# Kernel optimization log

Measured on AMD Instinct MI355X. Metric: run time of the kernel, lower is better.

The kernel has to match this reference:

```python
import jax, jax.numpy as jnp
import numpy as np

EPS = 1e-5
NUM_HEADS = 16


def activation_quant(x):
    # 8-bit activation quant with straight-through estimator
    scale = 127.0 / jnp.clip(jnp.max(jnp.abs(x), axis=-1, keepdims=True), 1e-5, None)
    y = jnp.clip(jnp.round(x * scale), -128.0, 127.0) / scale
    return x + jax.lax.stop_gradient(y - x)


def weight_quant(w):
    # ternary {-1,0,1} weight quant with STE
    scale = 1.0 / jnp.clip(jnp.mean(jnp.abs(w)), 1e-5, None)
    wq = jnp.clip(jnp.round(w * scale), -1.0, 1.0) / scale
    return w + jax.lax.stop_gradient(wq - w)


def bitlinear(x, w):
    # F.layer_norm(x, x.shape[1:]): normalize over ALL dims except batch, no affine
    axes = tuple(range(1, x.ndim))
    mu = jnp.mean(x, axis=axes, keepdims=True)
    var = jnp.var(x, axis=axes, keepdims=True)
    xn = (x - mu) * jax.lax.rsqrt(var + EPS)
    return jnp.einsum('bnd,od->bno', activation_quant(xn), weight_quant(w))


def layer_norm(x, gamma, beta):
    mu = jnp.mean(x, axis=-1, keepdims=True)
    var = jnp.var(x, axis=-1, keepdims=True)
    return (x - mu) * jax.lax.rsqrt(var + EPS) * gamma + beta


def setup_inputs() -> dict:
    key = jax.random.key(0)
    k0, k1, k2 = jax.random.split(key, 3)
    B, N, D = 2, 2048, 1024
    return {
        't': jnp.zeros((1,), jnp.float32),
        'x': jax.random.normal(k0, (B, N, D), jnp.float32),
        'w_qkv': jax.random.normal(k1, (3 * D, D), jnp.float32) * 0.02,
        'w_out': jax.random.normal(k2, (D, D), jnp.float32) * 0.02,
        'gamma': jnp.ones((D,), jnp.float32),
        'beta': jnp.zeros((D,), jnp.float32),
    }


def reference(t, x, w_qkv, w_out, gamma, beta):
    B, N, D = x.shape
    H = NUM_HEADS
    hd = D // H
    scale = hd ** -0.5
    h = layer_norm(x, gamma, beta)                     # [B,N,D]
    qkv = bitlinear(h, w_qkv).reshape(B, N, 3, H, hd)   # [B,N,3,H,hd]
    qkv = jnp.transpose(qkv, (2, 0, 3, 1, 4))           # [3,B,H,N,hd]
    q, k, v = qkv[0], qkv[1], qkv[2]
    attn = jax.nn.softmax(jnp.einsum('bhnd,bhmd->bhnm', q, k) * scale, axis=-1)
    out = jnp.einsum('bhnm,bhmd->bhnd', attn, v)        # [B,H,N,hd]
    out = jnp.transpose(out, (0, 2, 1, 3)).reshape(B, N, D)
    return bitlinear(out, w_out)
```

## Files before the change

kernel.cpp:

```cpp
#include <hip/hip_runtime.h>
#include <hip/hip_bf16.h>
#include <hip/hip_fp16.h>
#include <math.h>

typedef __hip_bfloat16 bf16;
typedef int   i32x4  __attribute__((ext_vector_type(4)));
typedef float f32x4  __attribute__((ext_vector_type(4)));
typedef float f32x16 __attribute__((ext_vector_type(16)));
typedef short bfx8   __attribute__((ext_vector_type(8)));

#define EPSV 1e-5f
#define NROWS 4096
#define DIM   1024
#define NSEQ  2048

__device__ __forceinline__ float ldv(const void* p, size_t i, int dt){
  if (dt == 0) return ((const float*)p)[i];
  if (dt == 1) return __bfloat162float(((const bf16*)p)[i]);
  return __half2float(((const __half*)p)[i]);
}

__device__ __forceinline__ void detect(const void* c0, const void* c1,
                                       int& dt, const void*& g, const void*& bta){
  unsigned u0 = *(const unsigned*)c0;
  int gfirst = (u0 != 0u) ? 1 : 0;
  g   = gfirst ? c0 : c1;
  bta = gfirst ? c1 : c0;
  unsigned short g0 = *(const unsigned short*)g;
  dt = (g0 == 0x3F80) ? 1 : ((g0 == 0x3C00) ? 2 : 0);
}

__device__ __forceinline__ float blk_sum(float v, float* sm){
  #pragma unroll
  for (int o = 32; o > 0; o >>= 1) v += __shfl_xor(v, o, 64);
  __syncthreads();
  if ((threadIdx.x & 63) == 0) sm[threadIdx.x >> 6] = v;
  __syncthreads();
  return sm[0] + sm[1] + sm[2] + sm[3];
}
__device__ __forceinline__ double blk_sum_d(double v, double* sm){
  #pragma unroll
  for (int o = 32; o > 0; o >>= 1) v += __shfl_xor(v, o, 64);
  __syncthreads();
  if ((threadIdx.x & 63) == 0) sm[threadIdx.x >> 6] = v;
  __syncthreads();
  return sm[0] + sm[1] + sm[2] + sm[3];
}
__device__ __forceinline__ float blk_max(float v, float* sm){
  #pragma unroll
  for (int o = 32; o > 0; o >>= 1) v = fmaxf(v, __shfl_xor(v, o, 64));
  __syncthreads();
  if ((threadIdx.x & 63) == 0) sm[threadIdx.x >> 6] = v;
  __syncthreads();
  return fmaxf(fmaxf(sm[0], sm[1]), fmaxf(sm[2], sm[3]));
}

__global__ __launch_bounds__(256) void ln_rows(const void* __restrict__ x,
                                               const void* __restrict__ c0,
                                               const void* __restrict__ c1,
                                               float* __restrict__ h,
                                               double* __restrict__ lnp){
  __shared__ float sm[4];
  __shared__ double smd[4];
  int dt; const void *g, *bta;
  detect(c0, c1, dt, g, bta);
  int row = blockIdx.x;
  int tid = threadIdx.x;
  float v[4]; float s = 0.f;
  float gmv[4], btv[4];
  if (dt == 0){
    float4 v4 = ((const float4*)x)[(size_t)row*256 + tid];
    v[0]=v4.x; v[1]=v4.y; v[2]=v4.z; v[3]=v4.w;
    float4 gm4 = ((const float4*)g)[tid];
    float4 bt4 = ((const float4*)bta)[tid];
    gmv[0]=gm4.x; gmv[1]=gm4.y; gmv[2]=gm4.z; gmv[3]=gm4.w;
    btv[0]=bt4.x; btv[1]=bt4.y; btv[2]=bt4.z; btv[3]=bt4.w;
  } else {
    size_t base = (size_t)row * DIM;
    #pragma unroll
    for (int i = 0; i < 4; ++i){
      v[i]   = ldv(x, base + 4*tid + i, dt);
      gmv[i] = ldv(g, 4*tid + i, dt);
      btv[i] = ldv(bta, 4*tid + i, dt);
    }
  }
  #pragma unroll
  for (int i = 0; i < 4; ++i) s += v[i];
  s = blk_sum(s, sm);
  float mu = s * (1.f/1024.f);
  float d2 = 0.f;
  #pragma unroll
  for (int i = 0; i < 4; ++i){ float d = v[i] - mu; d2 += d*d; }
  d2 = blk_sum(d2, sm);
  float rs = rsqrtf(d2 * (1.f/1024.f) + EPSV);
  float hv[4];
  #pragma unroll
  for (int i = 0; i < 4; ++i) hv[i] = (v[i]-mu)*rs*gmv[i] + btv[i];
  ((float4*)h)[(size_t)row*256 + tid] = make_float4(hv[0],hv[1],hv[2],hv[3]);
  double hs = 0.0, hq = 0.0;
  #pragma unroll
  for (int i = 0; i < 4; ++i){ hs += (double)hv[i]; hq += (double)hv[i]*(double)hv[i]; }
  hs = blk_sum_d(hs, smd);
  hq = blk_sum_d(hq, smd);
  if (tid == 0){ lnp[2*row] = hs; lnp[2*row + 1] = hq; }
}

__global__ __launch_bounds__(256) void abs_reduce_both(const void* __restrict__ wq,
                                                       const void* __restrict__ wo,
                                                       double* __restrict__ awp1,
                                                       double* __restrict__ awp2,
                                                       const void* __restrict__ c0,
                                                       const void* __restrict__ c1){
  __shared__ double smd[4];
  int dt; const void *g, *bta;
  detect(c0, c1, dt, g, bta);
  int blk = blockIdx.x;
  const void* w; int n; int nblk; int bi; double* part;
  if (blk < 512){ w = wq; n = 3*DIM*DIM; nblk = 512; bi = blk;      part = awp1; }
  else          { w = wo; n = DIM*DIM;   nblk = 128; bi = blk - 512; part = awp2; }
  double s = 0.0;
  if (dt == 0){
    const float4* w4 = (const float4*)w;
    int n4 = n >> 2;
    for (int i = bi*256 + threadIdx.x; i < n4; i += nblk*256){
      float4 v = w4[i];
      s += (double)(fabsf(v.x) + fabsf(v.y)) + (double)(fabsf(v.z) + fabsf(v.w));
    }
  } else {
    for (int i = bi*256 + threadIdx.x; i < n; i += nblk*256)
      s += (double)fabsf(ldv(w, i, dt));
  }
  s = blk_sum_d(s, smd);
  if (threadIdx.x == 0) part[bi] = s;
}

__global__ __launch_bounds__(256) void finalize1(float* acc,
                                                 const double* __restrict__ lnp,
                                                 const double* __restrict__ awp1,
                                                 const double* __restrict__ awp2){
  __shared__ double smd[4];
  int tid = threadIdx.x;
  double s0=0, q0=0, s1=0, q1=0, a1=0, a2=0;
  for (int i = tid; i < 2048; i += 256){
    s0 += lnp[2*i];          q0 += lnp[2*i + 1];
    s1 += lnp[2*(i+2048)];   q1 += lnp[2*(i+2048) + 1];
  }
  for (int i = tid; i < 512; i += 256) a1 += awp1[i];
  if (tid < 128) a2 = awp2[tid];
  s0 = blk_sum_d(s0, smd);  q0 = blk_sum_d(q0, smd);
  s1 = blk_sum_d(s1, smd);  q1 = blk_sum_d(q1, smd);
  a1 = blk_sum_d(a1, smd);  a2 = blk_sum_d(a2, smd);
  if (tid == 0){
    const double cnt = 2097152.0;
    double mu0 = s0/cnt, var0 = q0/cnt - mu0*mu0;
    double mu1 = s1/cnt, var1 = q1/cnt - mu1*mu1;
    acc[16] = (float)mu0; acc[17] = (float)(1.0 / sqrt(var0 + 1e-5));
    acc[18] = (float)mu1; acc[19] = (float)(1.0 / sqrt(var1 + 1e-5));
    acc[20] = (float)(1.0 / fmax(a1 / (3.0*1024.0*1024.0), 1e-5));
    acc[21] = (float)(1.0 / fmax(a2 / (1024.0*1024.0), 1e-5));
  }
}

__global__ __launch_bounds__(256) void finalize2(float* acc,
                                                 const double* __restrict__ atp){
  __shared__ double smd[4];
  int tid = threadIdx.x;
  double s0=0, q0=0, s1=0, q1=0;
  for (int i = tid; i < 512; i += 256){
    s0 += atp[2*i];          q0 += atp[2*i + 1];
    s1 += atp[2*(i+512)];    q1 += atp[2*(i+512) + 1];
  }
  s0 = blk_sum_d(s0, smd);  q0 = blk_sum_d(q0, smd);
  s1 = blk_sum_d(s1, smd);  q1 = blk_sum_d(q1, smd);
  if (tid == 0){
    const double cnt = 2097152.0;
    double mu0 = s0/cnt, var0 = q0/cnt - mu0*mu0;
    double mu1 = s1/cnt, var1 = q1/cnt - mu1*mu1;
    acc[22] = (float)mu0; acc[23] = (float)(1.0 / sqrt(var0 + 1e-5));
    acc[24] = (float)mu1; acc[25] = (float)(1.0 / sqrt(var1 + 1e-5));
  }
}

__global__ __launch_bounds__(256) void act_quant_i8(const float* __restrict__ buf,
                                                    signed char* __restrict__ qout,
                                                    float* __restrict__ rscale,
                                                    const float* __restrict__ acc,
                                                    int statOff){
  __shared__ float sm[4];
  int row = blockIdx.x;
  int b = row >> 11;
  float mu = acc[statOff + 2*b], rs = acc[statOff + 2*b + 1];
  int tid = threadIdx.x;
  float4 v4 = ((const float4*)buf)[(size_t)row*256 + tid];
  float v[4] = {(v4.x-mu)*rs, (v4.y-mu)*rs, (v4.z-mu)*rs, (v4.w-mu)*rs};
  float am = fmaxf(fmaxf(fabsf(v[0]), fabsf(v[1])), fmaxf(fabsf(v[2]), fabsf(v[3])));
  am = blk_max(am, sm);
  am = fmaxf(am, 1e-5f);
  float s127 = 127.f / am;
  unsigned pk = 0;
  #pragma unroll
  for (int i = 0; i < 4; ++i){
    float q = rintf(v[i] * s127);
    q = fminf(fmaxf(q, -128.f), 127.f);
    pk |= ((unsigned)(unsigned char)(signed char)q) << (8*i);
  }
  ((unsigned*)qout)[(size_t)row*256 + tid] = pk;
  if (tid == 0) rscale[row] = am * (1.f/127.f);
}

__global__ __launch_bounds__(256) void w_quant_both(const void* __restrict__ wqv,
                                                    const void* __restrict__ wov,
                                                    signed char* __restrict__ wqk,
                                                    signed char* __restrict__ wqo,
                                                    const float* __restrict__ acc,
                                                    const void* __restrict__ c0,
                                                    const void* __restrict__ c1){
  int dt; const void *g, *bta;
  detect(c0, c1, dt, g, bta);
  const int NQ4 = 786432;
  const int NT4 = 1048576;
  float s1 = acc[20], s2 = acc[21];
  if (dt == 0){
    for (int i = blockIdx.x*256 + threadIdx.x; i < NT4; i += gridDim.x*256){
      int inq = (i < NQ4);
      const float4* src = inq ? (const float4*)wqv : (const float4*)wov;
      unsigned* dst = inq ? (unsigned*)wqk : (unsigned*)wqo;
      int idx = inq ? i : (i - NQ4);
      float scale = inq ? s1 : s2;
      float4 v = src[idx];
      float vv[4] = {v.x, v.y, v.z, v.w};
      unsigned pk = 0;
      #pragma unroll
      for (int j = 0; j < 4; ++j){
        float q = rintf(vv[j] * scale);
        q = fminf(fmaxf(q, -1.f), 1.f);
        pk |= ((unsigned)(unsigned char)(signed char)q) << (8*j);
      }
      dst[idx] = pk;
    }
  } else {
    const int NQ = 3*DIM*DIM, NT = 4*DIM*DIM;
    for (int i = blockIdx.x*256 + threadIdx.x; i < NT; i += gridDim.x*256){
      int inq = (i < NQ);
      int idx = inq ? i : (i - NQ);
      float scale = inq ? s1 : s2;
      float q = rintf(ldv(inq ? wqv : wov, idx, dt) * scale);
      q = fminf(fmaxf(q, -1.f), 1.f);
      (inq ? wqk : wqo)[idx] = (signed char)q;
    }
  }
}

__global__ __launch_bounds__(256) void gemm_i8(const signed char* __restrict__ A,
                                               const signed char* __restrict__ W,
                                               const float* __restrict__ rscale,
                                               const float* __restrict__ acc, int sidx,
                                               float* __restrict__ Cf,
                                               bf16* __restrict__ Cb,
                                               int ldc, int writeBf, float q_prescale){
  __shared__ __attribute__((aligned(16))) signed char Asl[128][80];
  __shared__ __attribute__((aligned(16))) signed char Bsl[128][80];
  int tid = threadIdx.x, lane = tid & 63, w = tid >> 6;
  int wr = w >> 1, wc = w & 1;

  int nwgx = gridDim.x;
  int flat = blockIdx.y * nwgx + blockIdx.x;
  int nwg  = nwgx * gridDim.y;
  int cpx  = nwg >> 3;
  int swz  = (flat & 7) * cpx + (flat >> 3);
  int r0 = (swz / nwgx) * 128, o0 = (swz % nwgx) * 128;

  i32x4 zz = {0,0,0,0};
  i32x4 accv[4][4];
  #pragma unroll
  for (int m = 0; m < 4; ++m)
    #pragma unroll
    for (int n = 0; n < 4; ++n) accv[m][n] = zz;

  int sr0 = tid >> 2, sr1 = sr0 + 64;
  int sc  = (tid & 3) * 16;

  i32x4 a0, a1, b0, b1;
  a0 = *(const i32x4*)(A + (size_t)(r0 + sr0)*1024 + sc);
  a1 = *(const i32x4*)(A + (size_t)(r0 + sr1)*1024 + sc);
  b0 = *(const i32x4*)(W + (size_t)(o0 + sr0)*1024 + sc);
  b1 = *(const i32x4*)(W + (size_t)(o0 + sr1)*1024 + sc);

  for (int k0 = 0; k0 < 1024; k0 += 64){
    __syncthreads();
    *(i32x4*)&Asl[sr0][sc] = a0;
    *(i32x4*)&Asl[sr1][sc] = a1;
    *(i32x4*)&Bsl[sr0][sc] = b0;
    *(i32x4*)&Bsl[sr1][sc] = b1;
    __syncthreads();
    if (k0 + 64 < 1024){
      int kn = k0 + 64;
      a0 = *(const i32x4*)(A + (size_t)(r0 + sr0)*1024 + kn + sc);
      a1 = *(const i32x4*)(A + (size_t)(r0 + sr1)*1024 + kn + sc);
      b0 = *(const i32x4*)(W + (size_t)(o0 + sr0)*1024 + kn + sc);
      b1 = *(const i32x4*)(W + (size_t)(o0 + sr1)*1024 + kn + sc);
    }
    i32x4 af[4], bfr[4];
    #pragma unroll
    for (int m = 0; m < 4; ++m)
      af[m] = *(const i32x4*)&Asl[wr*64 + m*16 + (lane & 15)][(lane >> 4) * 16];
    #pragma unroll
    for (int n = 0; n < 4; ++n)
      bfr[n] = *(const i32x4*)&Bsl[wc*64 + n*16 + (lane & 15)][(lane >> 4) * 16];
    __builtin_amdgcn_s_setprio(1);
    #pragma unroll
    for (int m = 0; m < 4; ++m)
      #pragma unroll
      for (int n = 0; n < 4; ++n)
        accv[m][n] = __builtin_amdgcn_mfma_i32_16x16x64_i8(af[m], bfr[n], accv[m][n], 0, 0, 0);
    __builtin_amdgcn_s_setprio(0);
  }

  float wsc = acc[sidx];
  float cs = (o0 < 1024) ? q_prescale : 1.0f;
  float rf[4][4];
  #pragma unroll
  for (int m = 0; m < 4; ++m)
    #pragma unroll
    for (int r = 0; r < 4; ++r)
      rf[m][r] = rscale[r0 + wr*64 + m*16 + ((lane >> 4) << 2) + r] / wsc * cs;

  #pragma unroll
  for (int m = 0; m < 4; ++m)
    #pragma unroll
    for (int n = 0; n < 4; ++n)
      #pragma unroll
      for (int r = 0; r < 4; ++r){
        float val = (float)accv[m][n][r] * rf[m][r];
        size_t row = (size_t)(r0 + wr*64 + m*16 + ((lane >> 4) << 2) + r);
        int col = o0 + wc*64 + n*16 + (lane & 15);
        if (writeBf) Cb[row * ldc + col] = __float2bfloat16(val);
        else         Cf[row * ldc + col] = val;
      }
}

__global__ __launch_bounds__(128) void attn_mfma(const bf16* __restrict__ qkv,
                                                 float* __restrict__ out,
                                                 double* __restrict__ atp){
  __shared__ __attribute__((aligned(16))) unsigned short K_lds[64][64];
  __shared__ __attribute__((aligned(16))) unsigned short Vt_lds[64][64];
  __shared__ double smd[2];

  int tid = threadIdx.x, lane = tid & 63, w = tid >> 6;
  int l31 = lane & 31, hi = lane >> 5;

  int flat = blockIdx.y * 32 + blockIdx.x;
  int slot = flat & 7, idx = flat >> 3;
  int bh = slot * 4 + (idx >> 5);
  int qx = idx & 31;
  int b = bh >> 4, h = bh & 15;
  int n0 = qx * 64;
  const unsigned short* qg = (const unsigned short*)qkv;

  char* kB = (char*)K_lds;
  char* vB = (char*)Vt_lds;

  int qrow = b*NSEQ + n0 + w*32 + l31;
  bfx8 qf[4];
  #pragma unroll
  for (int kk = 0; kk < 4; ++kk)
    qf[kk] = *(const bfx8*)(qg + (size_t)qrow*3072 + h*64 + kk*16 + hi*8);

  float m_run = -INFINITY, l_run = 0.f;
  f32x16 acco[2];
  #pragma unroll
  for (int n = 0; n < 2; ++n)
    #pragma unroll
    for (int r = 0; r < 16; ++r) acco[n][r] = 0.f;

  int krow = tid & 63;
  int r2 = tid & 31, dw = tid >> 5;
  int k7 = krow & 7;

  bfx8 kc[4], vv[4];
  auto LOADT = [&](int kt){
    size_t kvb = (size_t)(b*NSEQ + kt*64);
    #pragma unroll
    for (int j = 0; j < 4; ++j)
      kc[j] = *(const bfx8*)(qg + (kvb + krow)*3072 + 1024 + h*64 + (w + 2*j)*8);
    vv[0] = *(const bfx8*)(qg + (kvb + 2*r2    )*3072 + 2048 + h*64 + dw*8);
    vv[1] = *(const bfx8*)(qg + (kvb + 2*r2 + 1)*3072 + 2048 + h*64 + dw*8);
    vv[2] = *(const bfx8*)(qg + (kvb + 2*r2    )*3072 + 2048 + h*64 + (dw+4)*8);
    vv[3] = *(const bfx8*)(qg + (kvb + 2*r2 + 1)*3072 + 2048 + h*64 + (dw+4)*8);
  };
  LOADT(0);

  for (int kt = 0; kt < NSEQ/64; ++kt){
    __syncthreads();
    #pragma unroll
    for (int j = 0; j < 4; ++j)
      *(bfx8*)(kB + krow*128 + (((w + 2*j) ^ k7) << 4)) = kc[j];
    #pragma unroll
    for (int u = 0; u < 8; ++u){
      unsigned w0 = (unsigned)(unsigned short)vv[0][u] |
                    ((unsigned)(unsigned short)vv[1][u] << 16);
      unsigned w1 = (unsigned)(unsigned short)vv[2][u] |
                    ((unsigned)(unsigned short)vv[3][u] << 16);
      *(unsigned*)(vB + (dw*8 + u)*128     + ((4*r2) ^ (u << 4))) = w0;
      *(unsigned*)(vB + ((dw+4)*8 + u)*128 + ((4*r2) ^ (u << 4))) = w1;
    }
    __syncthreads();
    if (kt + 1 < NSEQ/64) LOADT(kt + 1);

    f32x16 s0, s1;
    #pragma unroll
    for (int r = 0; r < 16; ++r){ s0[r] = 0.f; s1[r] = 0.f; }
    int q7 = l31 & 7;
    #pragma unroll
    for (int kk = 0; kk < 4; ++kk){
      bfx8 kb0 = *(const bfx8*)(kB + l31*128        + (((2*kk + hi) ^ q7) << 4));
      bfx8 kb1 = *(const bfx8*)(kB + (32 + l31)*128 + (((2*kk + hi) ^ q7) << 4));
      __builtin_amdgcn_s_setprio(1);
      s0 = __builtin_amdgcn_mfma_f32_32x32x16_bf16(kb0, qf[kk], s0, 0, 0, 0);
      s1 = __builtin_amdgcn_mfma_f32_32x32x16_bf16(kb1, qf[kk], s1, 0, 0, 0);
      __builtin_amdgcn_s_setprio(0);
    }

    float pm = s0[0];
    #pragma unroll
    for (int r = 1; r < 16; ++r) pm = fmaxf(pm, s0[r]);
    #pragma unroll
    for (int r = 0; r < 16; ++r) pm = fmaxf(pm, s1[r]);
    pm = fmaxf(pm, __shfl_xor(pm, 32, 64));
    if (__any(pm > m_run + 8.f)){
      float mnew = fmaxf(m_run, pm);
      float corr = __expf(m_run - mnew);
      m_run = mnew;
      l_run *= corr;
      #pragma unroll
      for (int r = 0; r < 16; ++r){
        float ca = __shfl(corr, (r & 3) + 8*(r >> 2) + 4*hi, 64);
        acco[0][r] *= ca; acco[1][r] *= ca;
      }
    }
    float ts = 0.f;
    #pragma unroll
    for (int r = 0; r < 16; ++r){
      s0[r] = __expf(s0[r] - m_run); ts += s0[r];
      s1[r] = __expf(s1[r] - m_run); ts += s1[r];
    }
    ts += __shfl_xor(ts, 32, 64);
    l_run += ts;

    #pragma unroll
    for (int kvb = 0; kvb < 2; ++kvb){
      const f32x16& s = kvb ? s1 : s0;
      #pragma unroll
      for (int kk2 = 0; kk2 < 2; ++kk2){
        int bse = kk2 * 8;
        unsigned wa, wb2, wc, wd;
        asm("v_cvt_pk_bf16_f32 %0, %1, %2" : "=v"(wa)  : "v"(s[bse+0]), "v"(s[bse+1]));
        asm("v_cvt_pk_bf16_f32 %0, %1, %2" : "=v"(wb2) : "v"(s[bse+4]), "v"(s[bse+5]));
        asm("v_cvt_pk_bf16_f32 %0, %1, %2" : "=v"(wc)  : "v"(s[bse+2]), "v"(s[bse+3]));
        asm("v_cvt_pk_bf16_f32 %0, %1, %2" : "=v"(wd)  : "v"(s[bse+6]), "v"(s[bse+7]));
        asm("v_permlane32_swap_b32 %0, %1" : "+v"(wa), "+v"(wb2));
        asm("v_permlane32_swap_b32 %0, %1" : "+v"(wc), "+v"(wd));
        unsigned pw[4] = {wa, wc, wb2, wd};
        bfx8 pa = *(bfx8*)pw;
        #pragma unroll
        for (int n = 0; n < 2; ++n){
          bfx8 vb = *(const bfx8*)(vB + (n*32 + l31)*128 +
                                   (((kvb*4 + kk2*2 + hi) ^ q7) << 4));
          __builtin_amdgcn_s_setprio(1);
          acco[n] = __builtin_amdgcn_mfma_f32_32x32x16_bf16(pa, vb, acco[n], 0, 0, 0);
          __builtin_amdgcn_s_setprio(0);
        }
      }
    }
  }

  float il = 1.f / l_run;
  float ila[16];
  #pragma unroll
  for (int r = 0; r < 16; ++r)
    ila[r] = __shfl(il, (r & 3) + 8*(r >> 2) + 4*hi, 64);
  double ssum = 0.0, ssq = 0.0;
  #pragma unroll
  for (int n = 0; n < 2; ++n)
    #pragma unroll
    for (int r = 0; r < 16; ++r){
      float o = acco[n][r] * ila[r];
      int orow = b*NSEQ + n0 + w*32 + (r & 3) + 8*(r >> 2) + 4*hi;
      out[(size_t)orow * DIM + h*64 + n*32 + l31] = o;
      ssum += (double)o; ssq += (double)o * (double)o;
    }
  #pragma unroll
  for (int o = 32; o > 0; o >>= 1){ ssum += __shfl_xor(ssum, o, 64); ssq += __shfl_xor(ssq, o, 64); }
  __syncthreads();
  if (lane == 0){ smd[w] = ssum; }
  __syncthreads();
  double tsum = smd[0] + smd[1];
  __syncthreads();
  if (lane == 0){ smd[w] = ssq; }
  __syncthreads();
  double tsq = smd[0] + smd[1];
  if (tid == 0){
    int bflat = bh * 32 + qx;
    atp[2*bflat] = tsum; atp[2*bflat + 1] = tsq;
  }
}

extern "C" void kernel_launch(void* const* d_in, const int* in_sizes, int n_in,
                              void* d_out, int out_size, void* d_ws, size_t ws_size,
                              hipStream_t stream) {
  int ix = -1, iwq = -1, iwo = -1, ig0 = -1, ig1 = -1;
  for (int i = 0; i < n_in; ++i){
    int s = in_sizes[i];
    if      (s == 4194304) ix  = i;
    else if (s == 3145728) iwq = i;
    else if (s == 1048576) iwo = i;
    else if (s == 1024){ if (ig0 < 0) ig0 = i; else ig1 = i; }
  }
  if (ix < 0 || iwq < 0 || iwo < 0 || ig0 < 0 || ig1 < 0){ ix=1; iwq=2; iwo=3; ig0=4; ig1=5; }
  const void* x     = d_in[ix];
  const void* w_qkv = d_in[iwq];
  const void* w_out = d_in[iwo];
  const void* g0    = d_in[ig0];
  const void* g1    = d_in[ig1];

  char* ws = (char*)d_ws;
  float*  acc     = (float*)ws;
  float*  rscale1 = (float*)(ws + 12288);
  float*  rscale2 = (float*)(ws + 28672);
  double* lnp     = (double*)(ws + 65536);
  double* awp1    = (double*)(ws + 131072);
  double* awp2    = (double*)(ws + 135168);
  double* atp     = (double*)(ws + 139264);
  float*        h      = (float*)      (ws + (1u<<20));
  signed char*  h_i8   = (signed char*)(ws + (17u<<20));
  signed char*  wqk_i8 = (signed char*)(ws + (21u<<20));
  signed char*  wqo_i8 = (signed char*)(ws + (24u<<20));
  bf16*         qkvb   = (bf16*)       (ws + (25u<<20));
  signed char*  a2_i8  = (signed char*)(ws + (49u<<20));
  float*        aout   = h;

  ln_rows<<<NROWS, 256, 0, stream>>>(x, g0, g1, h, lnp);
  abs_reduce_both<<<640, 256, 0, stream>>>(w_qkv, w_out, awp1, awp2, g0, g1);
  finalize1<<<1, 256, 0, stream>>>(acc, lnp, awp1, awp2);
  act_quant_i8<<<NROWS, 256, 0, stream>>>(h, h_i8, rscale1, acc, 16);
  w_quant_both<<<1024, 256, 0, stream>>>(w_qkv, w_out, wqk_i8, wqo_i8, acc, g0, g1);
  gemm_i8<<<dim3(24, 32), 256, 0, stream>>>(h_i8, wqk_i8, rscale1, acc, 20,
                                            nullptr, qkvb, 3072, 1, 0.125f);
  attn_mfma<<<dim3(32, 32), 128, 0, stream>>>(qkvb, aout, atp);
  finalize2<<<1, 256, 0, stream>>>(acc, atp);
  act_quant_i8<<<NROWS, 256, 0, stream>>>(aout, a2_i8, rscale2, acc, 22);
  gemm_i8<<<dim3(8, 32), 256, 0, stream>>>(a2_i8, wqo_i8, rscale2, acc, 21,
                                           (float*)d_out, nullptr, 1024, 0, 1.0f);
}
```

Baseline: 150.1 us.

## Split attention over two KV halves with a separate combine kernel

The attention kernel now splits the 2048 keys into two halves, doubling the grid. Each block writes an unnormalized bf16 partial output plus its running max and sum. A new combine kernel merges the two halves with rescaling, normalizes, writes the fp32 output and computes the block statistics needed later. The softmax also switches to exp2, with log2e folded into the QKV GEMM output scale, and the max reduction is restructured as a tree. This is meant to raise occupancy and parallelism in attention, at the cost of an extra kernel launch, extra partial-result memory traffic and bf16 rounding of the partial outputs.

```diff
diff --git a/kernel.cpp b/kernel.cpp
--- a/kernel.cpp
+++ b/kernel.cpp
@@ -14,10 +14,15 @@
 #define DIM   1024
 #define NSEQ  2048
 
+__device__ __forceinline__ float fexp2(float x){ return __builtin_amdgcn_exp2f(x); }
+
 __device__ __forceinline__ float ldv(const void* p, size_t i, int dt){
   if (dt == 0) return ((const float*)p)[i];
   if (dt == 1) return __bfloat162float(((const bf16*)p)[i]);
   return __half2float(((const __half*)p)[i]);
+}
+__device__ __forceinline__ float b2f(unsigned short u){
+  return __uint_as_float((unsigned)u << 16);
 }
 
 __device__ __forceinline__ void detect(const void* c0, const void* c1,
@@ -339,20 +344,20 @@
       }
 }
 
-__global__ __launch_bounds__(128) void attn_mfma(const bf16* __restrict__ qkv,
-                                                 float* __restrict__ out,
-                                                 double* __restrict__ atp){
+__global__ __launch_bounds__(128, 4) void attn_mfma(const bf16* __restrict__ qkv,
+                                                    unsigned short* __restrict__ op,
+                                                    float2* __restrict__ ml){
   __shared__ __attribute__((aligned(16))) unsigned short K_lds[64][64];
   __shared__ __attribute__((aligned(16))) unsigned short Vt_lds[64][64];
-  __shared__ double smd[2];
 
   int tid = threadIdx.x, lane = tid & 63, w = tid >> 6;
   int l31 = lane & 31, hi = lane >> 5;
 
   int flat = blockIdx.y * 32 + blockIdx.x;
   int slot = flat & 7, idx = flat >> 3;
-  int bh = slot * 4 + (idx >> 5);
-  int qx = idx & 31;
+  int bh = slot * 4 + (idx >> 6);
+  int rem = idx & 63;
+  int qx = rem >> 1, half = rem & 1;
   int b = bh >> 4, h = bh & 15;
   int n0 = qx * 64;
   const unsigned short* qg = (const unsigned short*)qkv;
@@ -376,10 +381,11 @@
   int krow = tid & 63;
   int r2 = tid & 31, dw = tid >> 5;
   int k7 = krow & 7;
+  int q7 = l31 & 7;
 
   bfx8 kc[4], vv[4];
   auto LOADT = [&](int kt){
-    size_t kvb = (size_t)(b*NSEQ + kt*64);
+    size_t kvb = (size_t)(b*NSEQ + half*1024 + kt*64);
     #pragma unroll
     for (int j = 0; j < 4; ++j)
       kc[j] = *(const bfx8*)(qg + (kvb + krow)*3072 + 1024 + h*64 + (w + 2*j)*8);
@@ -390,7 +396,7 @@
   };
   LOADT(0);
 
-  for (int kt = 0; kt < NSEQ/64; ++kt){
+  for (int kt = 0; kt < 16; ++kt){
     __syncthreads();
     #pragma unroll
     for (int j = 0; j < 4; ++j)
@@ -405,12 +411,11 @@
       *(unsigned*)(vB + ((dw+4)*8 + u)*128 + ((4*r2) ^ (u << 4))) = w1;
     }
     __syncthreads();
-    if (kt + 1 < NSEQ/64) LOADT(kt + 1);
+    if (kt + 1 < 16) LOADT(kt + 1);
 
     f32x16 s0, s1;
     #pragma unroll
     for (int r = 0; r < 16; ++r){ s0[r] = 0.f; s1[r] = 0.f; }
-    int q7 = l31 & 7;
     #pragma unroll
     for (int kk = 0; kk < 4; ++kk){
       bfx8 kb0 = *(const bfx8*)(kB + l31*128        + (((2*kk + hi) ^ q7) << 4));
@@ -421,15 +426,23 @@
       __builtin_amdgcn_s_setprio(0);
     }
 
-    float pm = s0[0];
-    #pragma unroll
-    for (int r = 1; r < 16; ++r) pm = fmaxf(pm, s0[r]);
-    #pragma unroll
-    for (int r = 0; r < 16; ++r) pm = fmaxf(pm, s1[r]);
+    float pa0 = fmaxf(s0[0], s0[1]),  pa1 = fmaxf(s0[2], s0[3]);
+    float pa2 = fmaxf(s0[4], s0[5]),  pa3 = fmaxf(s0[6], s0[7]);
+    #pragma unroll
+    for (int r = 8; r < 16; r += 4){
+      pa0 = fmaxf(pa0, fmaxf(s0[r], s0[r+1]));
+      pa1 = fmaxf(pa1, fmaxf(s0[r+2], s0[r+3]));
+    }
+    #pragma unroll
+    for (int r = 0; r < 16; r += 4){
+      pa2 = fmaxf(pa2, fmaxf(s1[r], s1[r+1]));
+      pa3 = fmaxf(pa3, fmaxf(s1[r+2], s1[r+3]));
+    }
+    float pm = fmaxf(fmaxf(pa0, pa1), fmaxf(pa2, pa3));
     pm = fmaxf(pm, __shfl_xor(pm, 32, 64));
-    if (__any(pm > m_run + 8.f)){
+    if (__any(pm > m_run + 11.5415605f)){
       float mnew = fmaxf(m_run, pm);
-      float corr = __expf(m_run - mnew);
+      float corr = fexp2(m_run - mnew);
       m_run = mnew;
       l_run *= corr;
       #pragma unroll
@@ -441,15 +454,15 @@
     float ts = 0.f;
     #pragma unroll
     for (int r = 0; r < 16; ++r){
-      s0[r] = __expf(s0[r] - m_run); ts += s0[r];
-      s1[r] = __expf(s1[r] - m_run); ts += s1[r];
+      s0[r] = fexp2(s0[r] - m_run); ts += s0[r];
+      s1[r] = fexp2(s1[r] - m_run); ts += s1[r];
     }
     ts += __shfl_xor(ts, 32, 64);
     l_run += ts;
 
     #pragma unroll
-    for (int kvb = 0; kvb < 2; ++kvb){
-      const f32x16& s = kvb ? s1 : s0;
+    for (int kvb2 = 0; kvb2 < 2; ++kvb2){
+      const f32x16& s = kvb2 ? s1 : s0;
       #pragma unroll
       for (int kk2 = 0; kk2 < 2; ++kk2){
         int bse = kk2 * 8;
@@ -461,48 +474,67 @@
         asm("v_permlane32_swap_b32 %0, %1" : "+v"(wa), "+v"(wb2));
         asm("v_permlane32_swap_b32 %0, %1" : "+v"(wc), "+v"(wd));
         unsigned pw[4] = {wa, wc, wb2, wd};
-        bfx8 pa = *(bfx8*)pw;
+        bfx8 pfr = *(bfx8*)pw;
         #pragma unroll
         for (int n = 0; n < 2; ++n){
           bfx8 vb = *(const bfx8*)(vB + (n*32 + l31)*128 +
-                                   (((kvb*4 + kk2*2 + hi) ^ q7) << 4));
+                                   (((kvb2*4 + kk2*2 + hi) ^ q7) << 4));
           __builtin_amdgcn_s_setprio(1);
-          acco[n] = __builtin_amdgcn_mfma_f32_32x32x16_bf16(pa, vb, acco[n], 0, 0, 0);
+          acco[n] = __builtin_amdgcn_mfma_f32_32x32x16_bf16(pfr, vb, acco[n], 0, 0, 0);
           __builtin_amdgcn_s_setprio(0);
         }
       }
     }
   }
 
-  float il = 1.f / l_run;
-  float ila[16];
-  #pragma unroll
-  for (int r = 0; r < 16; ++r)
-    ila[r] = __shfl(il, (r & 3) + 8*(r >> 2) + 4*hi, 64);
+  int rowbase = (b*NSEQ + n0 + w*32);
+  #pragma unroll
+  for (int n = 0; n < 2; ++n)
+    #pragma unroll
+    for (int r = 0; r < 16; ++r){
+      int rh = (rowbase + (r & 3) + 8*(r >> 2) + 4*hi) * 16 + h;
+      bf16 ob = __float2bfloat16(acco[n][r]);
+      op[(size_t)rh*128 + half*64 + n*32 + l31] = *reinterpret_cast<unsigned short*>(&ob);
+    }
+  if (hi == 0){
+    int rh = (rowbase + l31) * 16 + h;
+    ml[(size_t)rh*2 + half] = make_float2(m_run, l_run);
+  }
+}
+
+__global__ __launch_bounds__(256) void combine_attn(const unsigned short* __restrict__ op,
+                                                    const float2* __restrict__ ml,
+                                                    float* __restrict__ aout,
+                                                    double* __restrict__ atp){
+  __shared__ double smd[4];
+  int tid = threadIdx.x;
+  int rh = blockIdx.x*64 + (tid >> 2);
+  int d0 = (tid & 3) * 16;
+  const bfx8* o0p = (const bfx8*)(op + (size_t)rh*128 + d0);
+  const bfx8* o1p = (const bfx8*)(op + (size_t)rh*128 + 64 + d0);
+  bfx8 o0a = o0p[0], o0b = o0p[1];
+  bfx8 o1a = o1p[0], o1b = o1p[1];
+  float2 ml0 = ml[(size_t)rh*2], ml1 = ml[(size_t)rh*2 + 1];
+  float m = fmaxf(ml0.x, ml1.x);
+  float c0 = fexp2(ml0.x - m), c1 = fexp2(ml1.x - m);
+  float l = ml0.y*c0 + ml1.y*c1;
+  float inv = 1.f / l;
+  float ov[16];
+  #pragma unroll
+  for (int j = 0; j < 8; ++j){
+    ov[j]   = (b2f((unsigned short)o0a[j])*c0 + b2f((unsigned short)o1a[j])*c1) * inv;
+    ov[j+8] = (b2f((unsigned short)o0b[j])*c0 + b2f((unsigned short)o1b[j])*c1) * inv;
+  }
   double ssum = 0.0, ssq = 0.0;
   #pragma unroll
-  for (int n = 0; n < 2; ++n)
-    #pragma unroll
-    for (int r = 0; r < 16; ++r){
-      float o = acco[n][r] * ila[r];
-      int orow = b*NSEQ + n0 + w*32 + (r & 3) + 8*(r >> 2) + 4*hi;
-      out[(size_t)orow * DIM + h*64 + n*32 + l31] = o;
-      ssum += (double)o; ssq += (double)o * (double)o;
-    }
-  #pragma unroll
-  for (int o = 32; o > 0; o >>= 1){ ssum += __shfl_xor(ssum, o, 64); ssq += __shfl_xor(ssq, o, 64); }
-  __syncthreads();
-  if (lane == 0){ smd[w] = ssum; }
-  __syncthreads();
-  double tsum = smd[0] + smd[1];
-  __syncthreads();
-  if (lane == 0){ smd[w] = ssq; }
-  __syncthreads();
-  double tsq = smd[0] + smd[1];
-  if (tid == 0){
-    int bflat = bh * 32 + qx;
-    atp[2*bflat] = tsum; atp[2*bflat + 1] = tsq;
-  }
+  for (int j = 0; j < 16; ++j){ ssum += (double)ov[j]; ssq += (double)ov[j]*(double)ov[j]; }
+  float4* dst = (float4*)(aout + (size_t)rh*64 + d0);
+  #pragma unroll
+  for (int j = 0; j < 4; ++j)
+    dst[j] = make_float4(ov[4*j], ov[4*j+1], ov[4*j+2], ov[4*j+3]);
+  ssum = blk_sum_d(ssum, smd);
+  ssq  = blk_sum_d(ssq, smd);
+  if (tid == 0){ atp[2*blockIdx.x] = ssum; atp[2*blockIdx.x + 1] = ssq; }
 }
 
 extern "C" void kernel_launch(void* const* d_in, const int* in_sizes, int n_in,
@@ -537,6 +569,8 @@
   signed char*  wqo_i8 = (signed char*)(ws + (24u<<20));
   bf16*         qkvb   = (bf16*)       (ws + (25u<<20));
   signed char*  a2_i8  = (signed char*)(ws + (49u<<20));
+  float2*       mlbuf  = (float2*)     (ws + (53u<<20));
+  unsigned short* opart = (unsigned short*)h;
   float*        aout   = h;
 
   ln_rows<<<NROWS, 256, 0, stream>>>(x, g0, g1, h, lnp);
@@ -545,8 +579,9 @@
   act_quant_i8<<<NROWS, 256, 0, stream>>>(h, h_i8, rscale1, acc, 16);
   w_quant_both<<<1024, 256, 0, stream>>>(w_qkv, w_out, wqk_i8, wqo_i8, acc, g0, g1);
   gemm_i8<<<dim3(24, 32), 256, 0, stream>>>(h_i8, wqk_i8, rscale1, acc, 20,
-                                            nullptr, qkvb, 3072, 1, 0.125f);
-  attn_mfma<<<dim3(32, 32), 128, 0, stream>>>(qkvb, aout, atp);
+                                            nullptr, qkvb, 3072, 1, 0.125f * 1.44269504f);
+  attn_mfma<<<dim3(32, 64), 128, 0, stream>>>(qkvb, opart, mlbuf);
+  combine_attn<<<1024, 256, 0, stream>>>(opart, mlbuf, aout, atp);
   finalize2<<<1, 256, 0, stream>>>(acc, atp);
   act_quant_i8<<<NROWS, 256, 0, stream>>>(aout, a2_i8, rscale2, acc, 22);
   gemm_i8<<<dim3(8, 32), 256, 0, stream>>>(a2_i8, wqo_i8, rscale2, acc, 21,
```

Result: slower. 257.1 us (+71.3%).

## Store LN and attention outputs as bf16; use exp2 with folded log2e scale

Applied to the files above, without the earlier changes.

The layer-norm output and the attention output are now written as packed bf16 instead of fp32, and the activation-quant kernel reads them back as bf16. This halves the memory traffic through those two intermediates. The softmax now uses hardware exp2: log2(e) is folded into the QKV GEMM output scale and the rescale threshold is adjusted to match. The running-max reduction becomes a tree to shorten the dependency chain. The cost is bf16 rounding before the int8 activation quantization, which can shift some quantized values.

```diff
diff --git a/kernel.cpp b/kernel.cpp
--- a/kernel.cpp
+++ b/kernel.cpp
@@ -14,10 +14,19 @@
 #define DIM   1024
 #define NSEQ  2048
 
+__device__ __forceinline__ float fexp2(float x){ return __builtin_amdgcn_exp2f(x); }
+
 __device__ __forceinline__ float ldv(const void* p, size_t i, int dt){
   if (dt == 0) return ((const float*)p)[i];
   if (dt == 1) return __bfloat162float(((const bf16*)p)[i]);
   return __half2float(((const __half*)p)[i]);
+}
+__device__ __forceinline__ float b2f(unsigned u){
+  return __uint_as_float(u << 16);
+}
+__device__ __forceinline__ unsigned short f2bu(float f){
+  bf16 t = __float2bfloat16(f);
+  return *reinterpret_cast<unsigned short*>(&t);
 }
 
 __device__ __forceinline__ void detect(const void* c0, const void* c1,
@@ -58,7 +67,7 @@
 __global__ __launch_bounds__(256) void ln_rows(const void* __restrict__ x,
                                                const void* __restrict__ c0,
                                                const void* __restrict__ c1,
-                                               float* __restrict__ h,
+                                               unsigned short* __restrict__ h,
                                                double* __restrict__ lnp){
   __shared__ float sm[4];
   __shared__ double smd[4];
@@ -96,7 +105,9 @@
   float hv[4];
   #pragma unroll
   for (int i = 0; i < 4; ++i) hv[i] = (v[i]-mu)*rs*gmv[i] + btv[i];
-  ((float4*)h)[(size_t)row*256 + tid] = make_float4(hv[0],hv[1],hv[2],hv[3]);
+  unsigned p0 = (unsigned)f2bu(hv[0]) | ((unsigned)f2bu(hv[1]) << 16);
+  unsigned p1 = (unsigned)f2bu(hv[2]) | ((unsigned)f2bu(hv[3]) << 16);
+  ((uint2*)h)[(size_t)row*256 + tid] = make_uint2(p0, p1);
   double hs = 0.0, hq = 0.0;
   #pragma unroll
   for (int i = 0; i < 4; ++i){ hs += (double)hv[i]; hq += (double)hv[i]*(double)hv[i]; }
@@ -181,18 +192,22 @@
   }
 }
 
-__global__ __launch_bounds__(256) void act_quant_i8(const float* __restrict__ buf,
-                                                    signed char* __restrict__ qout,
-                                                    float* __restrict__ rscale,
-                                                    const float* __restrict__ acc,
-                                                    int statOff){
+__global__ __launch_bounds__(256) void act_quant_i8b(const unsigned short* __restrict__ buf,
+                                                     signed char* __restrict__ qout,
+                                                     float* __restrict__ rscale,
+                                                     const float* __restrict__ acc,
+                                                     int statOff){
   __shared__ float sm[4];
   int row = blockIdx.x;
   int b = row >> 11;
   float mu = acc[statOff + 2*b], rs = acc[statOff + 2*b + 1];
   int tid = threadIdx.x;
-  float4 v4 = ((const float4*)buf)[(size_t)row*256 + tid];
-  float v[4] = {(v4.x-mu)*rs, (v4.y-mu)*rs, (v4.z-mu)*rs, (v4.w-mu)*rs};
+  uint2 pk2 = ((const uint2*)buf)[(size_t)row*256 + tid];
+  float v[4];
+  v[0] = (b2f(pk2.x & 0xffffu) - mu) * rs;
+  v[1] = (b2f(pk2.x >> 16)     - mu) * rs;
+  v[2] = (b2f(pk2.y & 0xffffu) - mu) * rs;
+  v[3] = (b2f(pk2.y >> 16)     - mu) * rs;
   float am = fmaxf(fmaxf(fabsf(v[0]), fabsf(v[1])), fmaxf(fabsf(v[2]), fabsf(v[3])));
   am = blk_max(am, sm);
   am = fmaxf(am, 1e-5f);
@@ -340,7 +355,7 @@
 }
 
 __global__ __launch_bounds__(128) void attn_mfma(const bf16* __restrict__ qkv,
-                                                 float* __restrict__ out,
+                                                 unsigned short* __restrict__ out,
                                                  double* __restrict__ atp){
   __shared__ __attribute__((aligned(16))) unsigned short K_lds[64][64];
   __shared__ __attribute__((aligned(16))) unsigned short Vt_lds[64][64];
@@ -376,6 +391,7 @@
   int krow = tid & 63;
   int r2 = tid & 31, dw = tid >> 5;
   int k7 = krow & 7;
+  int q7 = l31 & 7;
 
   bfx8 kc[4], vv[4];
   auto LOADT = [&](int kt){
@@ -410,7 +426,6 @@
     f32x16 s0, s1;
     #pragma unroll
     for (int r = 0; r < 16; ++r){ s0[r] = 0.f; s1[r] = 0.f; }
-    int q7 = l31 & 7;
     #pragma unroll
     for (int kk = 0; kk < 4; ++kk){
       bfx8 kb0 = *(const bfx8*)(kB + l31*128        + (((2*kk + hi) ^ q7) << 4));
@@ -421,15 +436,23 @@
       __builtin_amdgcn_s_setprio(0);
     }
 
-    float pm = s0[0];
-    #pragma unroll
-    for (int r = 1; r < 16; ++r) pm = fmaxf(pm, s0[r]);
-    #pragma unroll
-    for (int r = 0; r < 16; ++r) pm = fmaxf(pm, s1[r]);
+    float pa0 = fmaxf(s0[0], s0[1]),  pa1 = fmaxf(s0[2], s0[3]);
+    float pa2 = fmaxf(s0[4], s0[5]),  pa3 = fmaxf(s0[6], s0[7]);
+    #pragma unroll
+    for (int r = 8; r < 16; r += 4){
+      pa0 = fmaxf(pa0, fmaxf(s0[r], s0[r+1]));
+      pa1 = fmaxf(pa1, fmaxf(s0[r+2], s0[r+3]));
+    }
+    #pragma unroll
+    for (int r = 0; r < 16; r += 4){
+      pa2 = fmaxf(pa2, fmaxf(s1[r], s1[r+1]));
+      pa3 = fmaxf(pa3, fmaxf(s1[r+2], s1[r+3]));
+    }
+    float pm = fmaxf(fmaxf(pa0, pa1), fmaxf(pa2, pa3));
     pm = fmaxf(pm, __shfl_xor(pm, 32, 64));
-    if (__any(pm > m_run + 8.f)){
+    if (__any(pm > m_run + 11.5415605f)){
       float mnew = fmaxf(m_run, pm);
-      float corr = __expf(m_run - mnew);
+      float corr = fexp2(m_run - mnew);
       m_run = mnew;
       l_run *= corr;
       #pragma unroll
@@ -441,15 +464,15 @@
     float ts = 0.f;
     #pragma unroll
     for (int r = 0; r < 16; ++r){
-      s0[r] = __expf(s0[r] - m_run); ts += s0[r];
-      s1[r] = __expf(s1[r] - m_run); ts += s1[r];
+      s0[r] = fexp2(s0[r] - m_run); ts += s0[r];
+      s1[r] = fexp2(s1[r] - m_run); ts += s1[r];
     }
     ts += __shfl_xor(ts, 32, 64);
     l_run += ts;
 
     #pragma unroll
-    for (int kvb = 0; kvb < 2; ++kvb){
-      const f32x16& s = kvb ? s1 : s0;
+    for (int kvb2 = 0; kvb2 < 2; ++kvb2){
+      const f32x16& s = kvb2 ? s1 : s0;
       #pragma unroll
       for (int kk2 = 0; kk2 < 2; ++kk2){
         int bse = kk2 * 8;
@@ -461,13 +484,13 @@
         asm("v_permlane32_swap_b32 %0, %1" : "+v"(wa), "+v"(wb2));
         asm("v_permlane32_swap_b32 %0, %1" : "+v"(wc), "+v"(wd));
         unsigned pw[4] = {wa, wc, wb2, wd};
-        bfx8 pa = *(bfx8*)pw;
+        bfx8 pfr = *(bfx8*)pw;
         #pragma unroll
         for (int n = 0; n < 2; ++n){
           bfx8 vb = *(const bfx8*)(vB + (n*32 + l31)*128 +
-                                   (((kvb*4 + kk2*2 + hi) ^ q7) << 4));
+                                   (((kvb2*4 + kk2*2 + hi) ^ q7) << 4));
           __builtin_amdgcn_s_setprio(1);
-          acco[n] = __builtin_amdgcn_mfma_f32_32x32x16_bf16(pa, vb, acco[n], 0, 0, 0);
+          acco[n] = __builtin_amdgcn_mfma_f32_32x32x16_bf16(pfr, vb, acco[n], 0, 0, 0);
           __builtin_amdgcn_s_setprio(0);
         }
       }
@@ -486,7 +509,7 @@
     for (int r = 0; r < 16; ++r){
       float o = acco[n][r] * ila[r];
       int orow = b*NSEQ + n0 + w*32 + (r & 3) + 8*(r >> 2) + 4*hi;
-      out[(size_t)orow * DIM + h*64 + n*32 + l31] = o;
+      out[(size_t)orow * DIM + h*64 + n*32 + l31] = f2bu(o);
       ssum += (double)o; ssq += (double)o * (double)o;
     }
   #pragma unroll
@@ -531,24 +554,24 @@
   double* awp1    = (double*)(ws + 131072);
   double* awp2    = (double*)(ws + 135168);
   double* atp     = (double*)(ws + 139264);
-  float*        h      = (float*)      (ws + (1u<<20));
+  unsigned short* h    = (unsigned short*)(ws + (1u<<20));
   signed char*  h_i8   = (signed char*)(ws + (17u<<20));
   signed char*  wqk_i8 = (signed char*)(ws + (21u<<20));
   signed char*  wqo_i8 = (signed char*)(ws + (24u<<20));
   bf16*         qkvb   = (bf16*)       (ws + (25u<<20));
   signed char*  a2_i8  = (signed char*)(ws + (49u<<20));
-  float*        aout   = h;
+  unsigned short* aout = h;
 
   ln_rows<<<NROWS, 256, 0, stream>>>(x, g0, g1, h, lnp);
   abs_reduce_both<<<640, 256, 0, stream>>>(w_qkv, w_out, awp1, awp2, g0, g1);
   finalize1<<<1, 256, 0, stream>>>(acc, lnp, awp1, awp2);
-  act_quant_i8<<<NROWS, 256, 0, stream>>>(h, h_i8, rscale1, acc, 16);
+  act_quant_i8b<<<NROWS, 256, 0, stream>>>(h, h_i8, rscale1, acc, 16);
   w_quant_both<<<1024, 256, 0, stream>>>(w_qkv, w_out, wqk_i8, wqo_i8, acc, g0, g1);
   gemm_i8<<<dim3(24, 32), 256, 0, stream>>>(h_i8, wqk_i8, rscale1, acc, 20,
-                                            nullptr, qkvb, 3072, 1, 0.125f);
+                                            nullptr, qkvb, 3072, 1, 0.125f * 1.44269504f);
   attn_mfma<<<dim3(32, 32), 128, 0, stream>>>(qkvb, aout, atp);
   finalize2<<<1, 256, 0, stream>>>(acc, atp);
-  act_quant_i8<<<NROWS, 256, 0, stream>>>(aout, a2_i8, rscale2, acc, 22);
+  act_quant_i8b<<<NROWS, 256, 0, stream>>>(aout, a2_i8, rscale2, acc, 22);
   gemm_i8<<<dim3(8, 32), 256, 0, stream>>>(a2_i8, wqo_i8, rscale2, acc, 21,
                                            (float*)d_out, nullptr, 1024, 0, 1.0f);
 }
```

After: 151.0 us. Within noise of the previous version (+0.6%).
